# Performance work log

Measured on AMD Instinct MI355X. Metric: run time of the kernel, lower is better.

## Reference

```python
import jax, jax.numpy as jnp
import numpy as np

N_EMBED = 1024
N_HEAD = 16
HEAD_DIM = N_EMBED // N_HEAD
N_CONTEXT = 2048
MASKED_BIAS = -10000.0


def setup_inputs() -> dict:
    key = jax.random.key(0)
    k1, k2, k3 = jax.random.split(key, 3)
    hidden_states = jax.random.normal(k1, (4, 2048, N_EMBED), dtype=jnp.float32)
    w_attn = jax.random.normal(k2, (N_EMBED, 3 * N_EMBED), dtype=jnp.float32) * 0.02
    b_attn = jnp.zeros((3 * N_EMBED,), dtype=jnp.float32)
    w_proj = jax.random.normal(k3, (N_EMBED, N_EMBED), dtype=jnp.float32) * 0.02
    b_proj = jnp.zeros((N_EMBED,), dtype=jnp.float32)
    return {"hidden_states": hidden_states, "w_attn": w_attn, "b_attn": b_attn,
            "w_proj": w_proj, "b_proj": b_proj}


def reference(hidden_states, w_attn, b_attn, w_proj, b_proj):
    B, S, E = hidden_states.shape
    # c_attn: Conv1D (x @ W + b)
    qkv = hidden_states @ w_attn + b_attn  # [B,S,3E]
    q, k, v = jnp.split(qkv, 3, axis=-1)
    # split heads -> [B,H,S,D]
    def split_heads(x):
        return x.reshape(B, S, N_HEAD, HEAD_DIM).transpose(0, 2, 1, 3)
    q = split_heads(q)
    k = split_heads(k)  # torch permutes key to [B,H,D,S]; we keep [B,H,S,D] and einsum
    v = split_heads(v)
    # attention scores scaled by sqrt(head_dim) (v.size(-1) == HEAD_DIM)
    w = jnp.einsum('bhqd,bhkd->bhqk', q, k) / jnp.float32(HEAD_DIM) ** 0.5
    causal = jnp.tril(jnp.ones((S, S), dtype=bool))  # bias buffer slice
    w = jnp.where(causal[None, None], w, jnp.asarray(MASKED_BIAS, w.dtype))
    w = jax.nn.softmax(w, axis=-1)  # dropout p=0 -> identity
    out = jnp.einsum('bhqk,bhkd->bhqd', w, v)  # [B,H,S,D]
    # merge heads
    out = out.transpose(0, 2, 1, 3).reshape(B, S, E)
    out = out @ w_proj + b_proj
    # key returned in torch layout [B,H,D,S]
    return out, k.transpose(0, 1, 3, 2), v
```

## Files before the change

### kernel.cpp

```cpp
#include <hip/hip_runtime.h>
#include <hip/hip_bf16.h>


typedef __attribute__((ext_vector_type(8))) short bfx8;
typedef __attribute__((ext_vector_type(4))) short bfx4;
typedef __attribute__((ext_vector_type(4))) float fx4;

#define MFMA(a, b, c) __builtin_amdgcn_mfma_f32_16x16x32_bf16(a, b, c, 0, 0, 0)

#define S_CTX 2048
#define NE 1024
#define NH 16
#define HD 64

#define QSCALE 0.18033688011112042f

__device__ __forceinline__ short f2bf(float f) {
  unsigned u = __float_as_uint(f);
  unsigned r = u + 0x7fffu + ((u >> 16) & 1u);
  return (short)(r >> 16);
}

__device__ __forceinline__ unsigned pkbf(float a, float b) {
  union {
    __hip_bfloat162 h;
    unsigned u;
  } c;
  c.h = __float22bfloat162_rn(make_float2(a, b));
  return c.u;
}

__device__ __forceinline__ void gload16(const void* g, void* l) {
  __builtin_amdgcn_global_load_lds(
      (const __attribute__((address_space(1))) unsigned int*)g,
      (__attribute__((address_space(3))) unsigned int*)l, 16, 0, 0);
}

__global__ __launch_bounds__(256) void convert_bf16_kernel(const float* __restrict__ in,
                                                           short* __restrict__ out) {
  size_t i = (size_t)blockIdx.x * 256 + threadIdx.x;
  fx4 v = *(const fx4*)(in + i * 4);
  bfx4 o;
#pragma unroll
  for (int j = 0; j < 4; ++j) o[j] = f2bf(v[j]);
  *(bfx4*)(out + i * 4) = o;
}

__global__ __launch_bounds__(256) void transpose_conv_kernel(const float* __restrict__ in,
                                                             short* __restrict__ out,
                                                             int R, int C) {
  __shared__ float tile[32][33];
  int tx = threadIdx.x, ty = threadIdx.y;
  int c0 = blockIdx.x * 32, r0 = blockIdx.y * 32;
#pragma unroll
  for (int i = 0; i < 4; ++i)
    tile[ty + i * 8][tx] = in[(size_t)(r0 + ty + i * 8) * C + c0 + tx];
  __syncthreads();
#pragma unroll
  for (int i = 0; i < 4; ++i)
    out[(size_t)(c0 + ty + i * 8) * R + r0 + tx] = f2bf(tile[tx][ty + i * 8]);
}

__device__ __forceinline__ void gemm128_mainloop(const short* __restrict__ A,
                                                 const short* __restrict__ B,
                                                 const int K, const int m0, const int n0,
                                                 short* As, short* Bs, fx4 acc[4][4]) {
  const int t = threadIdx.x;
  const int lane = t & 63, w = t >> 6;
  const int g = lane >> 4, li = lane & 15;
  const int wr = w >> 1, wc = w & 1;
  const int bsw = ((lane & 7) ^ (lane >> 3)) * 8;
  const int rowl = w * 8 + (lane >> 3);

  const short* ap[4];
  const short* bp[4];
  char* al[4];
  char* bl[4];
#pragma unroll
  for (int i = 0; i < 4; ++i) {
    const int row = i * 32 + rowl;
    ap[i] = A + (size_t)(m0 + row) * K + bsw;
    bp[i] = B + (size_t)(n0 + row) * K + bsw;
    al[i] = (char*)As + i * 4096 + w * 1024;
    bl[i] = (char*)Bs + i * 4096 + w * 1024;
  }

  const int nt = K >> 6;
  for (int tt = 0; tt < nt; ++tt) {
#pragma unroll
    for (int i = 0; i < 4; ++i) {
      gload16(ap[i], al[i]);
      gload16(bp[i], bl[i]);
      ap[i] += 64;
      bp[i] += 64;
    }
    __syncthreads();
#pragma unroll
    for (int ks = 0; ks < 2; ++ks) {
      bfx8 af[4], bf[4];
#pragma unroll
      for (int m = 0; m < 4; ++m) {
        const int R = wr * 64 + m * 16 + li;
        af[m] = *(const bfx8*)((const char*)As + R * 128 + (((ks * 4 + g) ^ (li & 7)) << 4));
      }
#pragma unroll
      for (int n = 0; n < 4; ++n) {
        const int R = wc * 64 + n * 16 + li;
        bf[n] = *(const bfx8*)((const char*)Bs + R * 128 + (((ks * 4 + g) ^ (li & 7)) << 4));
      }
#pragma unroll
      for (int m = 0; m < 4; ++m)
#pragma unroll
        for (int n = 0; n < 4; ++n)
          acc[m][n] = MFMA(af[m], bf[n], acc[m][n]);
    }
    __syncthreads();
  }
}

__global__ __launch_bounds__(256) void gemm_qkv_kernel(const short* __restrict__ X,
                                                       const short* __restrict__ WT,
                                                       const float* __restrict__ bias,
                                                       short* __restrict__ qbf,
                                                       short* __restrict__ kbf,
                                                       short* __restrict__ vT,
                                                       float* __restrict__ kT,
                                                       float* __restrict__ vout) {
  __shared__ short As[128 * 64];
  __shared__ short Bs[128 * 64];
  fx4 acc[4][4];
  const fx4 z = {0.f, 0.f, 0.f, 0.f};
#pragma unroll
  for (int m = 0; m < 4; ++m)
#pragma unroll
    for (int n = 0; n < 4; ++n) acc[m][n] = z;
  const int m0 = blockIdx.x * 128, n0 = blockIdx.y * 128;
  gemm128_mainloop(X, WT, 1024, m0, n0, As, Bs, acc);

  const int lane = threadIdx.x & 63, w = threadIdx.x >> 6;
  const int g = lane >> 4, li = lane & 15;
  const int wr = w >> 1, wc = w & 1;
  const int sec = n0 >> 10;
#pragma unroll
  for (int mf = 0; mf < 4; ++mf) {
#pragma unroll
    for (int nf = 0; nf < 4; ++nf) {
      const int mrow = m0 + wr * 64 + mf * 16 + g * 4;
      const int ncol = n0 + wc * 64 + nf * 16 + li;
      const float bv = bias[ncol];
      fx4 vv;
#pragma unroll
      for (int jj = 0; jj < 4; ++jj) vv[jj] = acc[mf][nf][jj] + bv;
      const int b = mrow >> 11, s = mrow & 2047;
      const int e = ncol & 1023, h = e >> 6, d = e & 63;
      const size_t bidx = ((size_t)((b * 16 + h) * 2048 + s)) * 64 + d;
      if (sec == 0) {
#pragma unroll
        for (int jj = 0; jj < 4; ++jj) qbf[bidx + (size_t)jj * 64] = f2bf(vv[jj] * QSCALE);
      } else if (sec == 1) {
#pragma unroll
        for (int jj = 0; jj < 4; ++jj) kbf[bidx + (size_t)jj * 64] = f2bf(vv[jj]);
        const size_t tb = ((size_t)((b * 16 + h) * 64 + d)) * 2048 + s;
        *(fx4*)(kT + tb) = vv;
      } else {
#pragma unroll
        for (int jj = 0; jj < 4; ++jj) vout[bidx + (size_t)jj * 64] = vv[jj];
        const size_t tb = ((size_t)((b * 16 + h) * 64 + d)) * 2048 + s;
        bfx4 pv;
#pragma unroll
        for (int jj = 0; jj < 4; ++jj) pv[jj] = f2bf(vv[jj]);
        *(bfx4*)(vT + tb) = pv;
      }
    }
  }
}

__global__ __launch_bounds__(256) void gemm_proj_kernel(const short* __restrict__ X,
                                                        const short* __restrict__ WT,
                                                        const float* __restrict__ bias,
                                                        float* __restrict__ out) {
  __shared__ short As[128 * 64];
  __shared__ short Bs[128 * 64];
  fx4 acc[4][4];
  const fx4 z = {0.f, 0.f, 0.f, 0.f};
#pragma unroll
  for (int m = 0; m < 4; ++m)
#pragma unroll
    for (int n = 0; n < 4; ++n) acc[m][n] = z;
  const int m0 = blockIdx.x * 128, n0 = blockIdx.y * 128;
  gemm128_mainloop(X, WT, 1024, m0, n0, As, Bs, acc);

  const int lane = threadIdx.x & 63, w = threadIdx.x >> 6;
  const int g = lane >> 4, li = lane & 15;
  const int wr = w >> 1, wc = w & 1;
#pragma unroll
  for (int mf = 0; mf < 4; ++mf) {
#pragma unroll
    for (int nf = 0; nf < 4; ++nf) {
      const int mrow = m0 + wr * 64 + mf * 16 + g * 4;
      const int ncol = n0 + wc * 64 + nf * 16 + li;
      const float bv = bias[ncol];
#pragma unroll
      for (int jj = 0; jj < 4; ++jj)
        out[(size_t)(mrow + jj) * 1024 + ncol] = acc[mf][nf][jj] + bv;
    }
  }
}

#define KSW(base, row, byte) ((char*)(base) + (row) * 128 + ((byte) ^ (((row) & 7) << 4)))

#define SOFTMAX_TILE(stv, accv, mrun, lrun, pAv, qm, diag)                    \
  {                                                                          \
    if (diag) {                                                              \
      const int qg = (qm) + li;                                              \
      _Pragma("unroll") for (int kt = 0; kt < 4; ++kt)                       \
          _Pragma("unroll") for (int jj = 0; jj < 4; ++jj) if (              \
              k0 + kt * 16 + g * 4 + jj > qg) stv[kt][jj] = -1e30f;          \
    }                                                                        \
    float pm = stv[0][0];                                                    \
    _Pragma("unroll") for (int kt = 0; kt < 4; ++kt)                         \
        _Pragma("unroll") for (int jj = 0; jj < 4; ++jj) pm =                \
            fmaxf(pm, stv[kt][jj]);                                          \
    if (!__all(pm <= (mrun) + 6.0f)) {                                       \
      pm = fmaxf(pm, __shfl_xor(pm, 16));                                    \
      pm = fmaxf(pm, __shfl_xor(pm, 32));                                    \
      const float mn = fmaxf((mrun), pm);                                    \
      const float rf = __builtin_amdgcn_exp2f((mrun) - mn);                  \
      (lrun) *= rf;                                                          \
      fx4 rfv;                                                               \
      _Pragma("unroll") for (int jj = 0; jj < 4; ++jj) rfv[jj] =             \
          __shfl(rf, g * 4 + jj);                                            \
      _Pragma("unroll") for (int dt = 0; dt < 4; ++dt) accv[dt] *= rfv;      \
      (mrun) = mn;                                                           \
    }                                                                        \
    union {                                                                  \
      bfx8 v;                                                                \
      unsigned u[4];                                                         \
    } pk_[2];                                                                \
    float ls = 0.f;                                                          \
    _Pragma("unroll") for (int kt = 0; kt < 4; ++kt) {                       \
      const float p0 = __builtin_amdgcn_exp2f(stv[kt][0] - (mrun));          \
      const float p1 = __builtin_amdgcn_exp2f(stv[kt][1] - (mrun));          \
      const float p2 = __builtin_amdgcn_exp2f(stv[kt][2] - (mrun));          \
      const float p3 = __builtin_amdgcn_exp2f(stv[kt][3] - (mrun));          \
      ls += (p0 + p1) + (p2 + p3);                                           \
      pk_[kt >> 1].u[(kt & 1) * 2 + 0] = pkbf(p0, p1);                       \
      pk_[kt >> 1].u[(kt & 1) * 2 + 1] = pkbf(p2, p3);                       \
    }                                                                        \
    ls += __shfl_xor(ls, 16);                                                \
    ls += __shfl_xor(ls, 32);                                                \
    (lrun) += ls;                                                            \
    pAv[0] = pk_[0].v;                                                       \
    pAv[1] = pk_[1].v;                                                       \
  }

__global__ __launch_bounds__(256, 4) void attn_kernel(const short* __restrict__ Q,
                                                      const short* __restrict__ Kc,
                                                      const short* __restrict__ VT,
                                                      short* __restrict__ O) {
  __shared__ short Ks[2][64 * 64];
  __shared__ short Vs[2][64 * 64];

  const int bh = blockIdx.x & 63;
  const int c = blockIdx.x >> 6;

  const int t = threadIdx.x;
  const int w = t >> 6;
  const int lane = t & 63;
  const int g = lane >> 4, li = lane & 15;

  const size_t hoff = (size_t)bh * (S_CTX * HD);
  const short* Qh = Q + hoff;
  const char* Khc = (const char*)(Kc + hoff);
  const char* Vhc = (const char*)(VT + hoff);

  const int lr = lane >> 3;
  const int bsw = ((lane & 7) ^ lr) * 16;
  const int rb0 = w * 16;

  const int qm0 = 64 * c + 16 * w;
  const int qm1 = 64 * (31 - c) + 16 * w;
  bfx8 qf0[2], qf1[2];
  qf0[0] = *(const bfx8*)(Qh + (size_t)(qm0 + li) * HD + g * 8);
  qf0[1] = *(const bfx8*)(Qh + (size_t)(qm0 + li) * HD + 32 + g * 8);
  qf1[0] = *(const bfx8*)(Qh + (size_t)(qm1 + li) * HD + g * 8);
  qf1[1] = *(const bfx8*)(Qh + (size_t)(qm1 + li) * HD + 32 + g * 8);

  fx4 acc0[4], acc1[4];
  const fx4 z = {0.f, 0.f, 0.f, 0.f};
#pragma unroll
  for (int dt = 0; dt < 4; ++dt) {
    acc0[dt] = z;
    acc1[dt] = z;
  }
  float m0 = -1e30f, l0 = 0.f, m1 = -1e30f, l1 = 0.f;

  const int tmax = 31 - c;

#define STAGE_TILE(k0s, buf)                                                        \
  {                                                                                 \
    _Pragma("unroll") for (int i = 0; i < 2; ++i) {                                 \
      const int rb = rb0 + i * 8;                                                   \
      const int row = rb + lr;                                                      \
      gload16(Khc + (size_t)((k0s) + row) * 128 + bsw, (char*)Ks[buf] + rb * 128);  \
      gload16(Vhc + (size_t)row * (S_CTX * 2) + (size_t)(k0s) * 2 + bsw,            \
              (char*)Vs[buf] + rb * 128);                                           \
    }                                                                               \
  }

  STAGE_TILE(0, 0);
  __syncthreads();

  for (int tt = 0; tt <= tmax; ++tt) {
    const int cur = tt & 1;
    const int k0 = tt * 64;
    if (tt < tmax) STAGE_TILE(k0 + 64, cur ^ 1);
    const bool act0 = (tt <= c);

    bfx8 pA0[2], pA1[2];
    {
      fx4 st[4] = {z, z, z, z};
#pragma unroll
      for (int h = 0; h < 2; ++h) {
        bfx8 kfh[4];
#pragma unroll
        for (int kt = 0; kt < 4; ++kt)
          kfh[kt] = *(const bfx8*)KSW(Ks[cur], kt * 16 + li, h * 64 + g * 16);
#pragma unroll
        for (int kt = 0; kt < 4; ++kt) st[kt] = MFMA(kfh[kt], qf1[h], st[kt]);
      }
      SOFTMAX_TILE(st, acc1, m1, l1, pA1, qm1, tt == tmax);
    }
    if (act0) {
      fx4 st[4] = {z, z, z, z};
#pragma unroll
      for (int h = 0; h < 2; ++h) {
        bfx8 kfh[4];
#pragma unroll
        for (int kt = 0; kt < 4; ++kt)
          kfh[kt] = *(const bfx8*)KSW(Ks[cur], kt * 16 + li, h * 64 + g * 16);
#pragma unroll
        for (int kt = 0; kt < 4; ++kt) st[kt] = MFMA(kfh[kt], qf0[h], st[kt]);
      }
      SOFTMAX_TILE(st, acc0, m0, l0, pA0, qm0, tt == c);
    }
#pragma unroll
    for (int kc = 0; kc < 2; ++kc) {
      bfx8 vfc[4];
#pragma unroll
      for (int dt = 0; dt < 4; ++dt) {
        const int row = dt * 16 + li;
        const bfx4 a = *(const bfx4*)KSW(Vs[cur], row, kc * 64 + g * 8);
        const bfx4 b = *(const bfx4*)KSW(Vs[cur], row, kc * 64 + 32 + g * 8);
        bfx8 vv;
#pragma unroll
        for (int j = 0; j < 4; ++j) {
          vv[j] = a[j];
          vv[j + 4] = b[j];
        }
        vfc[dt] = vv;
      }
#pragma unroll
      for (int dt = 0; dt < 4; ++dt) acc1[dt] = MFMA(pA1[kc], vfc[dt], acc1[dt]);
      if (act0) {
#pragma unroll
        for (int dt = 0; dt < 4; ++dt) acc0[dt] = MFMA(pA0[kc], vfc[dt], acc0[dt]);
      }
    }
    __syncthreads();
  }

  const int b = bh >> 4, h = bh & 15;
#pragma unroll
  for (int mf = 0; mf < 2; ++mf) {
    const int qm = mf ? qm1 : qm0;
    const float lr_ = mf ? l1 : l0;
    fx4 lv;
#pragma unroll
    for (int jj = 0; jj < 4; ++jj)
      lv[jj] = __builtin_amdgcn_rcpf(__shfl(lr_, g * 4 + jj));
#pragma unroll
    for (int dt = 0; dt < 4; ++dt)
#pragma unroll
      for (int jj = 0; jj < 4; ++jj) {
        const int s = qm + g * 4 + jj;
        const fx4 av = mf ? acc1[dt] : acc0[dt];
        O[((size_t)(b * S_CTX + s)) * NE + h * HD + dt * 16 + li] =
            f2bf(av[jj] * lv[jj]);
      }
  }
}

extern "C" void kernel_launch(void* const* d_in, const int* in_sizes, int n_in,
                              void* d_out, int out_size, void* d_ws, size_t ws_size,
                              hipStream_t stream) {
  const float* hs = (const float*)d_in[0];
  const float* w_attn = (const float*)d_in[1];
  const float* b_attn = (const float*)d_in[2];
  const float* w_proj = (const float*)d_in[3];
  const float* b_proj = (const float*)d_in[4];

  float* out = (float*)d_out;
  float* kT_out = out + 8388608;
  float* v_out = out + 2 * 8388608;

  char* ws = (char*)d_ws;
  short* xbf = (short*)ws;
  short* waT = (short*)(ws + 16777216);
  short* vTb = (short*)(ws + 23068672);
  short* qbf = (short*)(ws + 39845888);
  short* kbf = (short*)(ws + 56623104);
  short* wpT = (short*)(ws + 73400320);

  convert_bf16_kernel<<<8192, 256, 0, stream>>>(hs, xbf);
  transpose_conv_kernel<<<dim3(96, 32), dim3(32, 8), 0, stream>>>(w_attn, waT, 1024, 3072);
  transpose_conv_kernel<<<dim3(32, 32), dim3(32, 8), 0, stream>>>(w_proj, wpT, 1024, 1024);
  gemm_qkv_kernel<<<dim3(64, 24), 256, 0, stream>>>(xbf, waT, b_attn, qbf, kbf, vTb,
                                                    kT_out, v_out);
  attn_kernel<<<1024, 256, 0, stream>>>(qbf, kbf, vTb, xbf );
  gemm_proj_kernel<<<dim3(64, 8), 256, 0, stream>>>(xbf, wpT, b_proj, out);
}
```

Baseline: 176.1 us.

## Double-buffer LDS in GEMM mainloop and swap grid order for tile reuse

```diff
diff --git a/kernel.cpp b/kernel.cpp
--- a/kernel.cpp
+++ b/kernel.cpp
@@ -85,28 +85,43 @@
     bl[i] = (char*)Bs + i * 4096 + w * 1024;
   }
 
+#define GSTG(buf)                                     \
+  {                                                   \
+    _Pragma("unroll") for (int i = 0; i < 4; ++i) {   \
+      gload16(ap[i], al[i] + ((buf) << 14));          \
+      gload16(bp[i], bl[i] + ((buf) << 14));          \
+      ap[i] += 64;                                    \
+      bp[i] += 64;                                    \
+    }                                                 \
+  }
+
+  GSTG(0);
+
   const int nt = K >> 6;
   for (int tt = 0; tt < nt; ++tt) {
-#pragma unroll
-    for (int i = 0; i < 4; ++i) {
-      gload16(ap[i], al[i]);
-      gload16(bp[i], bl[i]);
-      ap[i] += 64;
-      bp[i] += 64;
-    }
-    __syncthreads();
+    const int cur = tt & 1;
+    if (tt + 1 < nt) {
+      GSTG(cur ^ 1);
+      asm volatile("s_waitcnt vmcnt(8)" ::: "memory");
+    } else {
+      asm volatile("s_waitcnt vmcnt(0)" ::: "memory");
+    }
+    __builtin_amdgcn_sched_barrier(0);
+    __builtin_amdgcn_s_barrier();
+    const char* Ab = (const char*)As + (cur << 14);
+    const char* Bb = (const char*)Bs + (cur << 14);
 #pragma unroll
     for (int ks = 0; ks < 2; ++ks) {
       bfx8 af[4], bf[4];
 #pragma unroll
       for (int m = 0; m < 4; ++m) {
         const int R = wr * 64 + m * 16 + li;
-        af[m] = *(const bfx8*)((const char*)As + R * 128 + (((ks * 4 + g) ^ (li & 7)) << 4));
+        af[m] = *(const bfx8*)(Ab + R * 128 + (((ks * 4 + g) ^ (li & 7)) << 4));
       }
 #pragma unroll
       for (int n = 0; n < 4; ++n) {
         const int R = wc * 64 + n * 16 + li;
-        bf[n] = *(const bfx8*)((const char*)Bs + R * 128 + (((ks * 4 + g) ^ (li & 7)) << 4));
+        bf[n] = *(const bfx8*)(Bb + R * 128 + (((ks * 4 + g) ^ (li & 7)) << 4));
       }
 #pragma unroll
       for (int m = 0; m < 4; ++m)
@@ -114,8 +129,10 @@
         for (int n = 0; n < 4; ++n)
           acc[m][n] = MFMA(af[m], bf[n], acc[m][n]);
     }
-    __syncthreads();
-  }
+    __builtin_amdgcn_sched_barrier(0);
+    __builtin_amdgcn_s_barrier();
+  }
+#undef GSTG
 }
 
 __global__ __launch_bounds__(256) void gemm_qkv_kernel(const short* __restrict__ X,
@@ -126,15 +143,15 @@
                                                        short* __restrict__ vT,
                                                        float* __restrict__ kT,
                                                        float* __restrict__ vout) {
-  __shared__ short As[128 * 64];
-  __shared__ short Bs[128 * 64];
+  __shared__ short As[2 * 128 * 64];
+  __shared__ short Bs[2 * 128 * 64];
   fx4 acc[4][4];
   const fx4 z = {0.f, 0.f, 0.f, 0.f};
 #pragma unroll
   for (int m = 0; m < 4; ++m)
 #pragma unroll
     for (int n = 0; n < 4; ++n) acc[m][n] = z;
-  const int m0 = blockIdx.x * 128, n0 = blockIdx.y * 128;
+  const int m0 = blockIdx.y * 128, n0 = blockIdx.x * 128;
   gemm128_mainloop(X, WT, 1024, m0, n0, As, Bs, acc);
 
   const int lane = threadIdx.x & 63, w = threadIdx.x >> 6;
@@ -179,15 +196,15 @@
                                                         const short* __restrict__ WT,
                                                         const float* __restrict__ bias,
                                                         float* __restrict__ out) {
-  __shared__ short As[128 * 64];
-  __shared__ short Bs[128 * 64];
+  __shared__ short As[2 * 128 * 64];
+  __shared__ short Bs[2 * 128 * 64];
   fx4 acc[4][4];
   const fx4 z = {0.f, 0.f, 0.f, 0.f};
 #pragma unroll
   for (int m = 0; m < 4; ++m)
 #pragma unroll
     for (int n = 0; n < 4; ++n) acc[m][n] = z;
-  const int m0 = blockIdx.x * 128, n0 = blockIdx.y * 128;
+  const int m0 = blockIdx.y * 128, n0 = blockIdx.x * 128;
   gemm128_mainloop(X, WT, 1024, m0, n0, As, Bs, acc);
 
   const int lane = threadIdx.x & 63, w = threadIdx.x >> 6;
@@ -415,8 +432,8 @@
   convert_bf16_kernel<<<8192, 256, 0, stream>>>(hs, xbf);
   transpose_conv_kernel<<<dim3(96, 32), dim3(32, 8), 0, stream>>>(w_attn, waT, 1024, 3072);
   transpose_conv_kernel<<<dim3(32, 32), dim3(32, 8), 0, stream>>>(w_proj, wpT, 1024, 1024);
-  gemm_qkv_kernel<<<dim3(64, 24), 256, 0, stream>>>(xbf, waT, b_attn, qbf, kbf, vTb,
+  gemm_qkv_kernel<<<dim3(24, 64), 256, 0, stream>>>(xbf, waT, b_attn, qbf, kbf, vTb,
                                                     kT_out, v_out);
   attn_kernel<<<1024, 256, 0, stream>>>(qbf, kbf, vTb, xbf );
-  gemm_proj_kernel<<<dim3(64, 8), 256, 0, stream>>>(xbf, wpT, b_proj, out);
-}
+  gemm_proj_kernel<<<dim3(8, 64), 256, 0, stream>>>(xbf, wpT, b_proj, out);
+}
```

After: 182.9 us. 1.04x slower.
